# Performance work log

Measured on AMD Instinct MI355X. Metric: run time of the kernel, lower is better.

Reference implementation:

```python
import jax, jax.numpy as jnp
import numpy as np

B, N, DIM = 1, 65536, 256
H, D, G = 8, 64, 64  # heads, dim_head, slice_num


def setup_inputs() -> dict:
    key = jax.random.key(0)
    ks = jax.random.split(key, 16)
    s = 0.02
    return {
        "x": jax.random.normal(ks[0], (B, N, DIM), jnp.float32),
        "Wx": jax.random.normal(ks[1], (H * D, DIM), jnp.float32) * s,
        "bx": jnp.zeros((H * D,), jnp.float32),
        "Wt1": jax.random.normal(ks[2], (G, D), jnp.float32) * s,
        "bt1": jnp.zeros((G,), jnp.float32),
        "Wt2": jax.random.normal(ks[3], (1, G), jnp.float32) * s,
        "bt2": jnp.zeros((1,), jnp.float32),
        "bias": jnp.ones((1, H, 1, 1), jnp.float32) * 0.5,
        "Ws": jax.random.normal(ks[4], (G, D), jnp.float32) * s,
        "bs": jnp.zeros((G,), jnp.float32),
        "Wq": jax.random.normal(ks[5], (D, D), jnp.float32) * s,
        "Wk": jax.random.normal(ks[6], (D, D), jnp.float32) * s,
        "Wv": jax.random.normal(ks[7], (D, D), jnp.float32) * s,
        "Wout": jax.random.normal(ks[8], (DIM, H * D), jnp.float32) * s,
        "bout": jnp.zeros((DIM,), jnp.float32),
        "u": jax.random.uniform(ks[9], (B, H, N, G), jnp.float32),
    }


def _gelu(t):
    return jax.nn.gelu(t, approximate=False)  # torch default exact GELU


def reference(x, Wx, bx, Wt1, bt1, Wt2, bt2, bias, Ws, bs, Wq, Wk, Wv, Wout, bout, u):
    b, n, _ = x.shape
    h, d, g = Wt1.shape[1] and bias.shape[1], Wq.shape[0], Ws.shape[0]
    # project and split heads: b n (h d) -> b h n d
    x_mid = (x @ Wx.T + bx).reshape(b, n, h, d).transpose(0, 2, 1, 3)
    # per-point temperature MLP + learned bias, clamped
    temp = _gelu(_gelu(x_mid @ Wt1.T + bt1) @ Wt2.T + bt2) + bias  # (b,h,n,1)
    temp = jnp.maximum(temp, 0.01)
    # gumbel-softmax slice routing (soft, hard=False)
    logits = x_mid @ Ws.T + bs  # (b,h,n,g)
    gnoise = -jnp.log(-jnp.log(u + 1e-8) + 1e-8)
    slice_weights = jax.nn.softmax((logits + gnoise) / temp, axis=-1)
    norm = slice_weights.sum(axis=2)  # (b,h,g)
    # gather-aggregate points into g slice tokens
    slice_tokens = jnp.einsum('bhnc,bhng->bhgc', x_mid, slice_weights)
    slice_tokens = slice_tokens / (norm[..., None] + 1e-5)
    # tiny g x g attention among slice tokens
    q = slice_tokens @ Wq.T
    k = slice_tokens @ Wk.T
    v = slice_tokens @ Wv.T
    attn = jax.nn.softmax((q @ k.transpose(0, 1, 3, 2)) * (d ** -0.5), axis=-1)
    out_slice = attn @ v  # (b,h,g,d)
    # scatter-combine back to points
    out = jnp.einsum('bhgd,bhng->bhnd', out_slice, slice_weights)
    out = out.transpose(0, 2, 1, 3).reshape(b, n, h * d)
    return out @ Wout.T + bout
```

## Files before the change

### kernel.cpp

```cpp
#include <hip/hip_runtime.h>
#include <math.h>

#define NPTS  65536
#define DIMX  256
#define NH    8
#define HDIM  512

typedef __attribute__((ext_vector_type(4))) float f32x4;
typedef __attribute__((ext_vector_type(8))) short short8;
typedef __attribute__((ext_vector_type(8))) unsigned short ushort8;
typedef __attribute__((ext_vector_type(4))) unsigned short us4;

__device__ __forceinline__ ushort f2bf(float f) {
    unsigned x = __float_as_uint(f);
    return (ushort)((x + 0x7fffu + ((x >> 16) & 1u)) >> 16);
}
__device__ __forceinline__ float bf2f(ushort u) {
    return __uint_as_float((unsigned)u << 16);
}
__device__ __forceinline__ float erf_fast(float x) {
    float ax = fabsf(x);
    float t  = __builtin_amdgcn_rcpf(1.0f + 0.3275911f * ax);
    float p  = fmaf(fmaf(fmaf(fmaf(1.061405429f, t, -1.453152027f), t,
                   1.421413741f), t, -0.284496736f), t, 0.254829592f) * t;
    float y  = 1.0f - p * __expf(-ax * ax);
    return copysignf(y, x);
}
__device__ __forceinline__ float gelu_fast(float x) {
    return 0.5f * x * (1.0f + erf_fast(x * 0.7071067811865476f));
}

__global__ __launch_bounds__(256)
void prep_kernel(const float* __restrict__ Wx, const float* __restrict__ Ws,
                 const float* __restrict__ Wt1,
                 ushort* __restrict__ Wxb, ushort* __restrict__ wb) {
    const int t = threadIdx.x;
    if (blockIdx.x < 64) {
        int idx = blockIdx.x * 2048 + t * 8;
        float4 a0 = *(const float4*)&Wx[idx];
        float4 a1 = *(const float4*)&Wx[idx + 4];
        ushort8 v = { f2bf(a0.x), f2bf(a0.y), f2bf(a0.z), f2bf(a0.w),
                      f2bf(a1.x), f2bf(a1.y), f2bf(a1.z), f2bf(a1.w) };
        *(ushort8*)&Wxb[idx] = v;
    } else {
        int idx = (blockIdx.x - 64) * 2048 + t * 8;
        int row = idx >> 6, col = idx & 63;
        const float* src = (row < 64) ? &Ws[row * 64 + col]
                                      : &Wt1[(row - 64) * 64 + col];
        float4 a0 = *(const float4*)src;
        float4 a1 = *(const float4*)(src + 4);
        ushort8 v = { f2bf(a0.x), f2bf(a0.y), f2bf(a0.z), f2bf(a0.w),
                      f2bf(a1.x), f2bf(a1.y), f2bf(a1.z), f2bf(a1.w) };
        *(ushort8*)&wb[idx] = v;
    }
}

__global__ __launch_bounds__(256)
void gemm_xmid_kernel(const float* __restrict__ A, const ushort* __restrict__ B,
                      const float* __restrict__ bias, ushort* __restrict__ C) {
    __shared__ __align__(16) ushort Al[128][64];
    __shared__ __align__(16) ushort Bl[128][64];
    const int m0 = blockIdx.x * 128, n0 = blockIdx.y * 128;
    const int t = threadIdx.x, l = t & 63, w = t >> 6;
    const int wr = w >> 1, wc = w & 1;
    const int lr = l & 15, lq = l >> 4;

    f32x4 acc[4][4];
    #pragma unroll
    for (int mi = 0; mi < 4; ++mi)
        #pragma unroll
        for (int ni = 0; ni < 4; ++ni) acc[mi][ni] = (f32x4){0.f, 0.f, 0.f, 0.f};

    for (int ks = 0; ks < 4; ++ks) {
        __syncthreads();
        #pragma unroll
        for (int i = 0; i < 4; ++i) {
            int idx = i * 256 + t;
            int row = idx >> 3, g = idx & 7;
            const float* ap = &A[(size_t)(m0 + row) * 256 + ks * 64 + g * 8];
            float4 a0 = *(const float4*)ap;
            float4 a1 = *(const float4*)(ap + 4);
            ushort8 av = { f2bf(a0.x), f2bf(a0.y), f2bf(a0.z), f2bf(a0.w),
                           f2bf(a1.x), f2bf(a1.y), f2bf(a1.z), f2bf(a1.w) };
            *(ushort8*)&Al[row][(g ^ (row & 7)) * 8] = av;
            ushort8 bv = *(const ushort8*)&B[(size_t)(n0 + row) * 256 + ks * 64 + g * 8];
            *(ushort8*)&Bl[row][(g ^ (row & 7)) * 8] = bv;
        }
        __syncthreads();
        #pragma unroll
        for (int kf = 0; kf < 2; ++kf) {
            short8 af[4], bfr[4];
            #pragma unroll
            for (int mi = 0; mi < 4; ++mi) {
                int row = wr * 64 + mi * 16 + lr, g = kf * 4 + lq;
                af[mi] = *(const short8*)&Al[row][(g ^ (row & 7)) * 8];
            }
            #pragma unroll
            for (int ni = 0; ni < 4; ++ni) {
                int row = wc * 64 + ni * 16 + lr, g = kf * 4 + lq;
                bfr[ni] = *(const short8*)&Bl[row][(g ^ (row & 7)) * 8];
            }
            #pragma unroll
            for (int mi = 0; mi < 4; ++mi)
                #pragma unroll
                for (int ni = 0; ni < 4; ++ni)
                    acc[mi][ni] = __builtin_amdgcn_mfma_f32_16x16x32_bf16(
                        af[mi], bfr[ni], acc[mi][ni], 0, 0, 0);
        }
    }
    #pragma unroll
    for (int ni = 0; ni < 4; ++ni) {
        int col = n0 + wc * 64 + ni * 16 + lr;
        float bb = bias[col];
        #pragma unroll
        for (int mi = 0; mi < 4; ++mi)
            #pragma unroll
            for (int j = 0; j < 4; ++j) {
                int row = m0 + wr * 64 + mi * 16 + lq * 4 + j;
                C[(size_t)row * 512 + col] = f2bf(acc[mi][ni][j] + bb);
            }
    }
}

__global__ __launch_bounds__(256)
void lgt1_mfma_kernel(const ushort* __restrict__ xmb,
                      const ushort* __restrict__ wb,
                      const float* __restrict__ bs,  const float* __restrict__ bt1,
                      const float* __restrict__ Wt2, const float* __restrict__ bt2,
                      const float* __restrict__ biasp,
                      const float* __restrict__ u,
                      ushort* __restrict__ swb) {
    __shared__ __align__(16) ushort Al[128][64];
    const int h = blockIdx.y, m0 = blockIdx.x * 128;
    const int t = threadIdx.x, l = t & 63, w = t >> 6;
    const int lr = l & 15, lq = l >> 4;
    const float LOG2E = 1.4426950408889634f;
    const float LN2   = 0.6931471805599453f;
    const float SH2   = 36.0673760222f;

    #pragma unroll
    for (int i = 0; i < 4; ++i) {
        int idx = i * 256 + t;
        int row = idx >> 3, g = idx & 7;
        ushort8 av = *(const ushort8*)&xmb[(size_t)(m0 + row) * 512 + h * 64 + g * 8];
        *(ushort8*)&Al[row][(g ^ (row & 7)) * 8] = av;
    }

    float uu0[4][4];
    #pragma unroll
    for (int jj = 0; jj < 4; ++jj) {
        const int n = m0 + w * 32 + lq * 4 + jj;
        const float* up = &u[((size_t)h * NPTS + n) * 64 + lr];
        #pragma unroll
        for (int ni = 0; ni < 4; ++ni) uu0[jj][ni] = up[ni * 16];
    }
    __syncthreads();

    f32x4 acc[2][8];
    #pragma unroll
    for (int mi = 0; mi < 2; ++mi)
        #pragma unroll
        for (int ni = 0; ni < 8; ++ni) acc[mi][ni] = (f32x4){0.f, 0.f, 0.f, 0.f};

    #pragma unroll
    for (int kf = 0; kf < 2; ++kf) {
        const int g = kf * 4 + lq;
        short8 af[2], bfr[8];
        #pragma unroll
        for (int mi = 0; mi < 2; ++mi) {
            int row = w * 32 + mi * 16 + lr;
            af[mi] = *(const short8*)&Al[row][(g ^ (row & 7)) * 8];
        }
        #pragma unroll
        for (int ni = 0; ni < 8; ++ni)
            bfr[ni] = *(const short8*)&wb[(size_t)(ni * 16 + lr) * 64 + g * 8];
        #pragma unroll
        for (int mi = 0; mi < 2; ++mi)
            #pragma unroll
            for (int ni = 0; ni < 8; ++ni)
                acc[mi][ni] = __builtin_amdgcn_mfma_f32_16x16x32_bf16(
                    af[mi], bfr[ni], acc[mi][ni], 0, 0, 0);
    }

    float uu1[4][4];
    #pragma unroll
    for (int jj = 0; jj < 4; ++jj) {
        const int n = m0 + w * 32 + 16 + lq * 4 + jj;
        const float* up = &u[((size_t)h * NPTS + n) * 64 + lr];
        #pragma unroll
        for (int ni = 0; ni < 4; ++ni) uu1[jj][ni] = up[ni * 16];
    }

    const float bt2v = bt2[0], biasph = biasp[h];
    float bsr[4], bt1r[4], wt2r[4];
    #pragma unroll
    for (int ni = 0; ni < 4; ++ni) {
        bsr[ni]  = bs [ni * 16 + lr];
        bt1r[ni] = bt1[ni * 16 + lr];
        wt2r[ni] = Wt2[ni * 16 + lr];
    }

    #pragma unroll
    for (int mi = 0; mi < 2; ++mi) {
        float ts[4];
        #pragma unroll
        for (int jj = 0; jj < 4; ++jj) {
            float s = 0.f;
            #pragma unroll
            for (int ni = 0; ni < 4; ++ni)
                s += gelu_fast(acc[mi][ni + 4][jj] + bt1r[ni]) * wt2r[ni];
            ts[jj] = s;
        }
        #pragma unroll
        for (int off = 1; off <= 8; off <<= 1) {
            #pragma unroll
            for (int jj = 0; jj < 4; ++jj) ts[jj] += __shfl_xor(ts[jj], off);
        }
        float invt[4], invt2[4];
        #pragma unroll
        for (int jj = 0; jj < 4; ++jj) {
            float tmp = gelu_fast(ts[jj] + bt2v) + biasph;
            tmp = fmaxf(tmp, 0.01f);
            invt[jj]  = __builtin_amdgcn_rcpf(tmp);
            invt2[jj] = invt[jj] * LOG2E;
        }
        float sv[4][4], ps[4] = {0.f, 0.f, 0.f, 0.f};
        #pragma unroll
        for (int jj = 0; jj < 4; ++jj) {
            #pragma unroll
            for (int ni = 0; ni < 4; ++ni) {
                float uuv = (mi == 0 ? uu0[jj][ni] : uu1[jj][ni]);
                float L1 = __log2f(uuv + 1e-8f);
                float inner = fmaf(-LN2, L1, 1e-8f);
                float L2v = __log2f(inner);
                float base = fmaf(acc[mi][ni][jj] + bsr[ni], invt2[jj], -SH2);
                sv[jj][ni] = __builtin_amdgcn_exp2f(fmaf(-invt[jj], L2v, base));
                ps[jj] += sv[jj][ni];
            }
        }
        #pragma unroll
        for (int off = 1; off <= 8; off <<= 1) {
            #pragma unroll
            for (int jj = 0; jj < 4; ++jj) ps[jj] += __shfl_xor(ps[jj], off);
        }
        #pragma unroll
        for (int jj = 0; jj < 4; ++jj) {
            const int n = m0 + w * 32 + mi * 16 + lq * 4 + jj;
            const float inv = __builtin_amdgcn_rcpf(ps[jj]);
            ushort* sp = &swb[(size_t)n * 512 + h * 64 + lr];
            #pragma unroll
            for (int ni = 0; ni < 4; ++ni)
                sp[ni * 16] = f2bf(sv[jj][ni] * inv);
        }
    }
}

__global__ __launch_bounds__(256)
void gather_mfma_kernel(const ushort* __restrict__ xmb, const ushort* __restrict__ swb,
                        float* __restrict__ stp, float* __restrict__ normp) {
    __shared__ __align__(16) ushort tile[2][64][128];
    ushort (* __restrict__ swT)[128] = tile[0];
    ushort (* __restrict__ xT )[128] = tile[1];
    const int h  = blockIdx.y;
    const int n0 = blockIdx.x * 1024;
    const int t  = threadIdx.x, l = t & 63, w = t >> 6;
    const int lr = l & 15, lq = l >> 4;
    const int gb = t & 7;
    const int ng = t >> 3;

    f32x4 acc[4][4];
    #pragma unroll
    for (int gi = 0; gi < 4; ++gi)
        #pragma unroll
        for (int ci = 0; ci < 4; ++ci) acc[gi][ci] = (f32x4){0.f, 0.f, 0.f, 0.f};
    float nrm8[8];
    #pragma unroll
    for (int j = 0; j < 8; ++j) nrm8[j] = 0.f;

    for (int r = 0; r < 8; ++r) {
        const int nt = n0 + r * 128;
        ushort8 sv[4], xv[4];
        #pragma unroll
        for (int i = 0; i < 4; ++i) {
            int n = nt + ng * 4 + i;
            sv[i] = *(const ushort8*)&swb[(size_t)n * 512 + h * 64 + gb * 8];
            xv[i] = *(const ushort8*)&xmb[(size_t)n * 512 + h * 64 + gb * 8];
        }
        __syncthreads();
        #pragma unroll
        for (int j = 0; j < 8; ++j) {
            int g   = gb * 8 + j;
            int swz = (ng >> 1) ^ (g & 7) ^ ((g >> 3) & 7);
            int off = swz * 8 + (ng & 1) * 4;
            us4 s4 = { sv[0][j], sv[1][j], sv[2][j], sv[3][j] };
            us4 x4 = { xv[0][j], xv[1][j], xv[2][j], xv[3][j] };
            *(us4*)&swT[g][off] = s4;
            *(us4*)&xT [g][off] = x4;
            nrm8[j] += (bf2f(sv[0][j]) + bf2f(sv[1][j]))
                     + (bf2f(sv[2][j]) + bf2f(sv[3][j]));
        }
        __syncthreads();
        short8 af[4], bfr[4];
        #pragma unroll
        for (int gi = 0; gi < 4; ++gi) {
            int g   = gi * 16 + lr;
            int swz = (w * 4 + lq) ^ (g & 7) ^ ((g >> 3) & 7);
            af[gi]  = *(const short8*)&swT[g][swz * 8];
            bfr[gi] = *(const short8*)&xT [g][swz * 8];
        }
        #pragma unroll
        for (int gi = 0; gi < 4; ++gi)
            #pragma unroll
            for (int ci = 0; ci < 4; ++ci)
                acc[gi][ci] = __builtin_amdgcn_mfma_f32_16x16x32_bf16(
                    af[gi], bfr[ci], acc[gi][ci], 0, 0, 0);
    }

    float* sred = (float*)tile;
    const size_t stbase = ((size_t)h * 64 + blockIdx.x) * 4096;
    #pragma unroll
    for (int half = 0; half < 2; ++half) {
        __syncthreads();
        #pragma unroll
        for (int gg = 0; gg < 2; ++gg) {
            int gi = half * 2 + gg;
            #pragma unroll
            for (int ci = 0; ci < 4; ++ci)
                #pragma unroll
                for (int j = 0; j < 4; ++j)
                    sred[(w * 32 + gg * 16 + lq * 4 + j) * 64 + ci * 16 + lr]
                        = acc[gi][ci][j];
        }
        __syncthreads();
        #pragma unroll
        for (int i = 0; i < 8; ++i) {
            int e = i * 256 + t;
            float s = (sred[e] + sred[2048 + e]) + (sred[4096 + e] + sred[6144 + e]);
            stp[stbase + half * 2048 + e] = s;
        }
    }

    __syncthreads();
    float* narr = (float*)tile;
    #pragma unroll
    for (int j = 0; j < 8; ++j) narr[ng * 64 + gb * 8 + j] = nrm8[j];
    __syncthreads();
    if (t < 64) {
        float s = 0.f;
        #pragma unroll 8
        for (int k = 0; k < 32; ++k) s += narr[k * 64 + t];
        normp[((size_t)h * 64 + blockIdx.x) * 64 + t] = s;
    }
}

__global__ __launch_bounds__(256)
void reduce_st_kernel(const float* __restrict__ stp, const float* __restrict__ normp,
                      float* __restrict__ st_red, float* __restrict__ nrm) {
    const int h = blockIdx.x;
    const int e = blockIdx.y * 256 + threadIdx.x;
    float s = 0.f;
    #pragma unroll 8
    for (int ch = 0; ch < 64; ++ch)
        s += stp[((size_t)h * 64 + ch) * 4096 + e];
    st_red[(size_t)h * 4096 + e] = s;
    if (blockIdx.y == 0 && threadIdx.x < 64) {
        float ns = 0.f;
        #pragma unroll 8
        for (int ch = 0; ch < 64; ++ch)
            ns += normp[((size_t)h * 64 + ch) * 64 + threadIdx.x];
        nrm[h * 64 + threadIdx.x] = ns + 1e-5f;
    }
}

__global__ __launch_bounds__(256)
void attn_small_kernel(const float* __restrict__ st_red, const float* __restrict__ nrm,
                       const float* __restrict__ Wq, const float* __restrict__ Wk,
                       const float* __restrict__ Wv, float* __restrict__ osl) {
    __shared__ float st[64][68];
    __shared__ float ql[64][68];
    __shared__ float kl[64][68];
    __shared__ float vl[64][68];
    __shared__ float sc[64][68];
    __shared__ float nl[64];
    const int h = blockIdx.x;
    const int t = threadIdx.x;

    if (t < 64) nl[t] = nrm[h * 64 + t];
    __syncthreads();
    for (int e = t; e < 4096; e += 256)
        st[e>>6][e&63] = st_red[(size_t)h * 4096 + e] / nl[e>>6];
    __syncthreads();
    for (int e = t; e < 4096; e += 256) {
        int g = e >> 6, dd = e & 63;
        float aq = 0.f, ak = 0.f, av = 0.f;
        for (int cc = 0; cc < 64; ++cc) {
            float sv = st[g][cc];
            aq = fmaf(sv, Wq[dd*64 + cc], aq);
            ak = fmaf(sv, Wk[dd*64 + cc], ak);
            av = fmaf(sv, Wv[dd*64 + cc], av);
        }
        ql[g][dd] = aq; kl[g][dd] = ak; vl[g][dd] = av;
    }
    __syncthreads();
    for (int e = t; e < 4096; e += 256) {
        int g = e >> 6, gp = e & 63;
        float s = 0.f;
        for (int dd = 0; dd < 64; ++dd) s = fmaf(ql[g][dd], kl[gp][dd], s);
        sc[g][gp] = s * 0.125f;
    }
    __syncthreads();
    if (t < 64) {
        float m = -1e30f;
        for (int j = 0; j < 64; ++j) m = fmaxf(m, sc[t][j]);
        float ssum = 0.f;
        for (int j = 0; j < 64; ++j) { float p = expf(sc[t][j] - m); sc[t][j] = p; ssum += p; }
        float inv = 1.f / ssum;
        for (int j = 0; j < 64; ++j) sc[t][j] *= inv;
    }
    __syncthreads();
    for (int e = t; e < 4096; e += 256) {
        int g = e >> 6, dd = e & 63;
        float s = 0.f;
        for (int gp = 0; gp < 64; ++gp) s = fmaf(sc[g][gp], vl[gp][dd], s);
        osl[(size_t)h * 4096 + e] = s;
    }
}

__global__ __launch_bounds__(256)
void fold_kernel(const float* __restrict__ osl, const float* __restrict__ Wout,
                 ushort* __restrict__ Mtb) {
    __shared__ float os[64][65];
    __shared__ float wl[128][65];
    const int h  = blockIdx.x;
    const int i0 = blockIdx.y * 128;
    const int t  = threadIdx.x;
    for (int e = t; e < 4096; e += 256) os[e>>6][e&63] = osl[(size_t)h * 4096 + e];
    for (int e = t; e < 8192; e += 256) {
        int i = e >> 6, d = e & 63;
        wl[i][d] = Wout[(size_t)(i0 + i) * HDIM + h * 64 + d];
    }
    __syncthreads();
    const int g = t & 63, iq = t >> 6;
    #pragma unroll 4
    for (int k = 0; k < 32; ++k) {
        int i = iq * 32 + k;
        float s = 0.f;
        #pragma unroll
        for (int d = 0; d < 64; ++d) s = fmaf(os[g][d], wl[i][d], s);
        Mtb[(size_t)(i0 + i) * HDIM + h * 64 + g] = f2bf(s);
    }
}

__global__ __launch_bounds__(256)
void gemm_out_kernel(const ushort* __restrict__ A, const ushort* __restrict__ B,
                     const float* __restrict__ bias, float* __restrict__ C) {
    __shared__ __align__(16) ushort Al[128][64];
    __shared__ __align__(16) ushort Bl[128][64];
    const int m0 = blockIdx.x * 128, n0 = blockIdx.y * 128;
    const int t = threadIdx.x, l = t & 63, w = t >> 6;
    const int wr = w >> 1, wc = w & 1;
    const int lr = l & 15, lq = l >> 4;

    f32x4 acc[4][4];
    #pragma unroll
    for (int mi = 0; mi < 4; ++mi)
        #pragma unroll
        for (int ni = 0; ni < 4; ++ni) acc[mi][ni] = (f32x4){0.f, 0.f, 0.f, 0.f};

    for (int ks = 0; ks < 8; ++ks) {
        __syncthreads();
        #pragma unroll
        for (int i = 0; i < 4; ++i) {
            int idx = i * 256 + t;
            int row = idx >> 3, g = idx & 7;
            ushort8 av = *(const ushort8*)&A[(size_t)(m0 + row) * 512 + ks * 64 + g * 8];
            *(ushort8*)&Al[row][(g ^ (row & 7)) * 8] = av;
            ushort8 bv = *(const ushort8*)&B[(size_t)(n0 + row) * 512 + ks * 64 + g * 8];
            *(ushort8*)&Bl[row][(g ^ (row & 7)) * 8] = bv;
        }
        __syncthreads();
        #pragma unroll
        for (int kf = 0; kf < 2; ++kf) {
            short8 af[4], bfr[4];
            #pragma unroll
            for (int mi = 0; mi < 4; ++mi) {
                int row = wr * 64 + mi * 16 + lr, g = kf * 4 + lq;
                af[mi] = *(const short8*)&Al[row][(g ^ (row & 7)) * 8];
            }
            #pragma unroll
            for (int ni = 0; ni < 4; ++ni) {
                int row = wc * 64 + ni * 16 + lr, g = kf * 4 + lq;
                bfr[ni] = *(const short8*)&Bl[row][(g ^ (row & 7)) * 8];
            }
            #pragma unroll
            for (int mi = 0; mi < 4; ++mi)
                #pragma unroll
                for (int ni = 0; ni < 4; ++ni)
                    acc[mi][ni] = __builtin_amdgcn_mfma_f32_16x16x32_bf16(
                        af[mi], bfr[ni], acc[mi][ni], 0, 0, 0);
        }
    }
    #pragma unroll
    for (int ni = 0; ni < 4; ++ni) {
        int col = n0 + wc * 64 + ni * 16 + lr;
        float bb = bias[col];
        #pragma unroll
        for (int mi = 0; mi < 4; ++mi)
            #pragma unroll
            for (int j = 0; j < 4; ++j) {
                int row = m0 + wr * 64 + mi * 16 + lq * 4 + j;
                C[(size_t)row * 256 + col] = acc[mi][ni][j] + bb;
            }
    }
}

extern "C" void kernel_launch(void* const* d_in, const int* in_sizes, int n_in,
                              void* d_out, int out_size, void* d_ws, size_t ws_size,
                              hipStream_t stream) {
    const float* x    = (const float*)d_in[0];
    const float* Wx   = (const float*)d_in[1];
    const float* bx   = (const float*)d_in[2];
    const float* Wt1  = (const float*)d_in[3];
    const float* bt1  = (const float*)d_in[4];
    const float* Wt2  = (const float*)d_in[5];
    const float* bt2  = (const float*)d_in[6];
    const float* biasp= (const float*)d_in[7];
    const float* Ws   = (const float*)d_in[8];
    const float* bs   = (const float*)d_in[9];
    const float* Wq   = (const float*)d_in[10];
    const float* Wk   = (const float*)d_in[11];
    const float* Wv   = (const float*)d_in[12];
    const float* Wout = (const float*)d_in[13];
    const float* bout = (const float*)d_in[14];
    const float* u    = (const float*)d_in[15];
    float* out = (float*)d_out;

    float*  stp    = (float*)d_ws;
    float*  normp  = stp    + (size_t)NH * 64 * 4096;
    float*  st_red = normp  + (size_t)NH * 64 * 64;
    float*  nrm    = st_red + (size_t)NH * 4096;
    float*  osl    = nrm    + (size_t)NH * 64;
    ushort* wb     = (ushort*)(osl + (size_t)NH * 4096);
    ushort* Wxb    = wb  + (size_t)128 * 64;
    ushort* Mtb    = Wxb + (size_t)HDIM * DIMX;
    ushort* xmb    = Mtb + (size_t)DIMX * HDIM;
    ushort* swb    = xmb + (size_t)NPTS * HDIM;

    prep_kernel<<<68, 256, 0, stream>>>(Wx, Ws, Wt1, Wxb, wb);
    gemm_xmid_kernel<<<dim3(512, 4), 256, 0, stream>>>(x, Wxb, bx, xmb);
    lgt1_mfma_kernel<<<dim3(512, 8), 256, 0, stream>>>(xmb, wb, bs, bt1,
                                                       Wt2, bt2, biasp, u, swb);
    gather_mfma_kernel<<<dim3(64, 8), 256, 0, stream>>>(xmb, swb, stp, normp);
    reduce_st_kernel<<<dim3(8, 16), 256, 0, stream>>>(stp, normp, st_red, nrm);
    attn_small_kernel<<<8, 256, 0, stream>>>(st_red, nrm, Wq, Wk, Wv, osl);
    fold_kernel<<<dim3(8, 2), 256, 0, stream>>>(osl, Wout, Mtb);
    gemm_out_kernel<<<dim3(512, 2), 256, 0, stream>>>(swb, Mtb, bout, out);
}
```

Before: 266.0 us.

## Fuse x_mid projection GEMM with slice-logit/temperature kernel via LDS handoff

Merges the x_mid GEMM and the per-head logits/temperature/softmax kernel into one launch. Each block computes a 128x128 x_mid tile (two heads), stages it in LDS, writes it coalesced to global memory, and then runs the second MFMA stage for both heads directly from LDS. This removes the re-read of x_mid from global memory and one kernel launch. The x_mid store also becomes row-coalesced 16-byte writes instead of scattered 2-byte ones. The cost is higher register pressure and fewer blocks in flight for the softmax stage.

```diff
diff --git a/kernel.cpp b/kernel.cpp
--- a/kernel.cpp
+++ b/kernel.cpp
@@ -56,14 +56,23 @@
 }
 
 __global__ __launch_bounds__(256)
-void gemm_xmid_kernel(const float* __restrict__ A, const ushort* __restrict__ B,
-                      const float* __restrict__ bias, ushort* __restrict__ C) {
-    __shared__ __align__(16) ushort Al[128][64];
-    __shared__ __align__(16) ushort Bl[128][64];
-    const int m0 = blockIdx.x * 128, n0 = blockIdx.y * 128;
+void xmid_lgt1_kernel(const float* __restrict__ A, const ushort* __restrict__ B,
+                      const float* __restrict__ bias,
+                      const ushort* __restrict__ wb,
+                      const float* __restrict__ bs,  const float* __restrict__ bt1,
+                      const float* __restrict__ Wt2, const float* __restrict__ bt2,
+                      const float* __restrict__ biasp,
+                      const float* __restrict__ u,
+                      ushort* __restrict__ xmb, ushort* __restrict__ swb) {
+    __shared__ __align__(16) ushort pool[2][128][64];
+    const int hp = blockIdx.y;
+    const int m0 = blockIdx.x * 128, n0 = hp * 128;
     const int t = threadIdx.x, l = t & 63, w = t >> 6;
     const int wr = w >> 1, wc = w & 1;
     const int lr = l & 15, lq = l >> 4;
+    const float LOG2E = 1.4426950408889634f;
+    const float LN2   = 0.6931471805599453f;
+    const float SH2   = 36.0673760222f;
 
     f32x4 acc[4][4];
     #pragma unroll
@@ -82,9 +91,9 @@
             float4 a1 = *(const float4*)(ap + 4);
             ushort8 av = { f2bf(a0.x), f2bf(a0.y), f2bf(a0.z), f2bf(a0.w),
                            f2bf(a1.x), f2bf(a1.y), f2bf(a1.z), f2bf(a1.w) };
-            *(ushort8*)&Al[row][(g ^ (row & 7)) * 8] = av;
+            *(ushort8*)&pool[0][row][(g ^ (row & 7)) * 8] = av;
             ushort8 bv = *(const ushort8*)&B[(size_t)(n0 + row) * 256 + ks * 64 + g * 8];
-            *(ushort8*)&Bl[row][(g ^ (row & 7)) * 8] = bv;
+            *(ushort8*)&pool[1][row][(g ^ (row & 7)) * 8] = bv;
         }
         __syncthreads();
         #pragma unroll
@@ -93,12 +102,12 @@
             #pragma unroll
             for (int mi = 0; mi < 4; ++mi) {
                 int row = wr * 64 + mi * 16 + lr, g = kf * 4 + lq;
-                af[mi] = *(const short8*)&Al[row][(g ^ (row & 7)) * 8];
+                af[mi] = *(const short8*)&pool[0][row][(g ^ (row & 7)) * 8];
             }
             #pragma unroll
             for (int ni = 0; ni < 4; ++ni) {
                 int row = wc * 64 + ni * 16 + lr, g = kf * 4 + lq;
-                bfr[ni] = *(const short8*)&Bl[row][(g ^ (row & 7)) * 8];
+                bfr[ni] = *(const short8*)&pool[1][row][(g ^ (row & 7)) * 8];
             }
             #pragma unroll
             for (int mi = 0; mi < 4; ++mi)
@@ -108,90 +117,32 @@
                         af[mi], bfr[ni], acc[mi][ni], 0, 0, 0);
         }
     }
+
+    __syncthreads();
+    ushort (* __restrict__ Xl)[128] = (ushort (*)[128])(&pool[0][0][0]);
     #pragma unroll
     for (int ni = 0; ni < 4; ++ni) {
-        int col = n0 + wc * 64 + ni * 16 + lr;
-        float bb = bias[col];
+        int colL = wc * 64 + ni * 16 + lr;
+        float bb = bias[n0 + colL];
+        int gg = colL >> 3, c7 = colL & 7;
         #pragma unroll
         for (int mi = 0; mi < 4; ++mi)
             #pragma unroll
             for (int j = 0; j < 4; ++j) {
-                int row = m0 + wr * 64 + mi * 16 + lq * 4 + j;
-                C[(size_t)row * 512 + col] = f2bf(acc[mi][ni][j] + bb);
-            }
-    }
-}
-
-__global__ __launch_bounds__(256)
-void lgt1_mfma_kernel(const ushort* __restrict__ xmb,
-                      const ushort* __restrict__ wb,
-                      const float* __restrict__ bs,  const float* __restrict__ bt1,
-                      const float* __restrict__ Wt2, const float* __restrict__ bt2,
-                      const float* __restrict__ biasp,
-                      const float* __restrict__ u,
-                      ushort* __restrict__ swb) {
-    __shared__ __align__(16) ushort Al[128][64];
-    const int h = blockIdx.y, m0 = blockIdx.x * 128;
-    const int t = threadIdx.x, l = t & 63, w = t >> 6;
-    const int lr = l & 15, lq = l >> 4;
-    const float LOG2E = 1.4426950408889634f;
-    const float LN2   = 0.6931471805599453f;
-    const float SH2   = 36.0673760222f;
-
-    #pragma unroll
-    for (int i = 0; i < 4; ++i) {
-        int idx = i * 256 + t;
-        int row = idx >> 3, g = idx & 7;
-        ushort8 av = *(const ushort8*)&xmb[(size_t)(m0 + row) * 512 + h * 64 + g * 8];
-        *(ushort8*)&Al[row][(g ^ (row & 7)) * 8] = av;
-    }
-
-    float uu0[4][4];
-    #pragma unroll
-    for (int jj = 0; jj < 4; ++jj) {
-        const int n = m0 + w * 32 + lq * 4 + jj;
-        const float* up = &u[((size_t)h * NPTS + n) * 64 + lr];
-        #pragma unroll
-        for (int ni = 0; ni < 4; ++ni) uu0[jj][ni] = up[ni * 16];
-    }
-    __syncthreads();
-
-    f32x4 acc[2][8];
-    #pragma unroll
-    for (int mi = 0; mi < 2; ++mi)
-        #pragma unroll
-        for (int ni = 0; ni < 8; ++ni) acc[mi][ni] = (f32x4){0.f, 0.f, 0.f, 0.f};
-
-    #pragma unroll
-    for (int kf = 0; kf < 2; ++kf) {
-        const int g = kf * 4 + lq;
-        short8 af[2], bfr[8];
-        #pragma unroll
-        for (int mi = 0; mi < 2; ++mi) {
-            int row = w * 32 + mi * 16 + lr;
-            af[mi] = *(const short8*)&Al[row][(g ^ (row & 7)) * 8];
-        }
-        #pragma unroll
-        for (int ni = 0; ni < 8; ++ni)
-            bfr[ni] = *(const short8*)&wb[(size_t)(ni * 16 + lr) * 64 + g * 8];
-        #pragma unroll
-        for (int mi = 0; mi < 2; ++mi)
-            #pragma unroll
-            for (int ni = 0; ni < 8; ++ni)
-                acc[mi][ni] = __builtin_amdgcn_mfma_f32_16x16x32_bf16(
-                    af[mi], bfr[ni], acc[mi][ni], 0, 0, 0);
-    }
-
-    float uu1[4][4];
-    #pragma unroll
-    for (int jj = 0; jj < 4; ++jj) {
-        const int n = m0 + w * 32 + 16 + lq * 4 + jj;
-        const float* up = &u[((size_t)h * NPTS + n) * 64 + lr];
-        #pragma unroll
-        for (int ni = 0; ni < 4; ++ni) uu1[jj][ni] = up[ni * 16];
-    }
-
-    const float bt2v = bt2[0], biasph = biasp[h];
+                int row = wr * 64 + mi * 16 + lq * 4 + j;
+                Xl[row][(gg ^ (row & 7)) * 8 + c7] = f2bf(acc[mi][ni][j] + bb);
+            }
+    }
+    __syncthreads();
+    #pragma unroll
+    for (int i = 0; i < 8; ++i) {
+        int e = i * 256 + t;
+        int row = e >> 4, gg = e & 15;
+        ushort8 v = *(const ushort8*)&Xl[row][(gg ^ (row & 7)) * 8];
+        *(ushort8*)&xmb[(size_t)(m0 + row) * 512 + n0 + gg * 8] = v;
+    }
+
+    const float bt2v = bt2[0];
     float bsr[4], bt1r[4], wt2r[4];
     #pragma unroll
     for (int ni = 0; ni < 4; ++ni) {
@@ -201,56 +152,96 @@
     }
 
     #pragma unroll
-    for (int mi = 0; mi < 2; ++mi) {
-        float ts[4];
-        #pragma unroll
-        for (int jj = 0; jj < 4; ++jj) {
-            float s = 0.f;
-            #pragma unroll
-            for (int ni = 0; ni < 4; ++ni)
-                s += gelu_fast(acc[mi][ni + 4][jj] + bt1r[ni]) * wt2r[ni];
-            ts[jj] = s;
-        }
-        #pragma unroll
-        for (int off = 1; off <= 8; off <<= 1) {
-            #pragma unroll
-            for (int jj = 0; jj < 4; ++jj) ts[jj] += __shfl_xor(ts[jj], off);
-        }
-        float invt[4], invt2[4];
-        #pragma unroll
-        for (int jj = 0; jj < 4; ++jj) {
-            float tmp = gelu_fast(ts[jj] + bt2v) + biasph;
-            tmp = fmaxf(tmp, 0.01f);
-            invt[jj]  = __builtin_amdgcn_rcpf(tmp);
-            invt2[jj] = invt[jj] * LOG2E;
-        }
-        float sv[4][4], ps[4] = {0.f, 0.f, 0.f, 0.f};
-        #pragma unroll
-        for (int jj = 0; jj < 4; ++jj) {
-            #pragma unroll
-            for (int ni = 0; ni < 4; ++ni) {
-                float uuv = (mi == 0 ? uu0[jj][ni] : uu1[jj][ni]);
-                float L1 = __log2f(uuv + 1e-8f);
-                float inner = fmaf(-LN2, L1, 1e-8f);
-                float L2v = __log2f(inner);
-                float base = fmaf(acc[mi][ni][jj] + bsr[ni], invt2[jj], -SH2);
-                sv[jj][ni] = __builtin_amdgcn_exp2f(fmaf(-invt[jj], L2v, base));
-                ps[jj] += sv[jj][ni];
-            }
-        }
-        #pragma unroll
-        for (int off = 1; off <= 8; off <<= 1) {
-            #pragma unroll
-            for (int jj = 0; jj < 4; ++jj) ps[jj] += __shfl_xor(ps[jj], off);
-        }
-        #pragma unroll
-        for (int jj = 0; jj < 4; ++jj) {
-            const int n = m0 + w * 32 + mi * 16 + lq * 4 + jj;
-            const float inv = __builtin_amdgcn_rcpf(ps[jj]);
-            ushort* sp = &swb[(size_t)n * 512 + h * 64 + lr];
-            #pragma unroll
-            for (int ni = 0; ni < 4; ++ni)
-                sp[ni * 16] = f2bf(sv[jj][ni] * inv);
+    for (int hh = 0; hh < 2; ++hh) {
+        const int h = hp * 2 + hh;
+        const float biasph = biasp[h];
+
+        f32x4 acc2[2][8];
+        #pragma unroll
+        for (int mi = 0; mi < 2; ++mi)
+            #pragma unroll
+            for (int ni = 0; ni < 8; ++ni) acc2[mi][ni] = (f32x4){0.f, 0.f, 0.f, 0.f};
+
+        #pragma unroll
+        for (int kf = 0; kf < 2; ++kf) {
+            const int g = kf * 4 + lq;
+            short8 af[2], bfr[8];
+            #pragma unroll
+            for (int mi = 0; mi < 2; ++mi) {
+                int row = w * 32 + mi * 16 + lr;
+                int gg = hh * 8 + g;
+                af[mi] = *(const short8*)&Xl[row][(gg ^ (row & 7)) * 8];
+            }
+            #pragma unroll
+            for (int ni = 0; ni < 8; ++ni)
+                bfr[ni] = *(const short8*)&wb[(size_t)(ni * 16 + lr) * 64 + g * 8];
+            #pragma unroll
+            for (int mi = 0; mi < 2; ++mi)
+                #pragma unroll
+                for (int ni = 0; ni < 8; ++ni)
+                    acc2[mi][ni] = __builtin_amdgcn_mfma_f32_16x16x32_bf16(
+                        af[mi], bfr[ni], acc2[mi][ni], 0, 0, 0);
+        }
+
+        #pragma unroll
+        for (int mi = 0; mi < 2; ++mi) {
+            float uu[4][4];
+            #pragma unroll
+            for (int jj = 0; jj < 4; ++jj) {
+                const int n = m0 + w * 32 + mi * 16 + lq * 4 + jj;
+                const float* up = &u[((size_t)h * NPTS + n) * 64 + lr];
+                #pragma unroll
+                for (int ni = 0; ni < 4; ++ni) uu[jj][ni] = up[ni * 16];
+            }
+            float ts[4];
+            #pragma unroll
+            for (int jj = 0; jj < 4; ++jj) {
+                float s = 0.f;
+                #pragma unroll
+                for (int ni = 0; ni < 4; ++ni)
+                    s += gelu_fast(acc2[mi][ni + 4][jj] + bt1r[ni]) * wt2r[ni];
+                ts[jj] = s;
+            }
+            #pragma unroll
+            for (int off = 1; off <= 8; off <<= 1) {
+                #pragma unroll
+                for (int jj = 0; jj < 4; ++jj) ts[jj] += __shfl_xor(ts[jj], off);
+            }
+            float invt[4], invt2[4];
+            #pragma unroll
+            for (int jj = 0; jj < 4; ++jj) {
+                float tmp = gelu_fast(ts[jj] + bt2v) + biasph;
+                tmp = fmaxf(tmp, 0.01f);
+                invt[jj]  = __builtin_amdgcn_rcpf(tmp);
+                invt2[jj] = invt[jj] * LOG2E;
+            }
+            float sv[4][4], ps[4] = {0.f, 0.f, 0.f, 0.f};
+            #pragma unroll
+            for (int jj = 0; jj < 4; ++jj) {
+                #pragma unroll
+                for (int ni = 0; ni < 4; ++ni) {
+                    float L1 = __log2f(uu[jj][ni] + 1e-8f);
+                    float inner = fmaf(-LN2, L1, 1e-8f);
+                    float L2v = __log2f(inner);
+                    float base = fmaf(acc2[mi][ni][jj] + bsr[ni], invt2[jj], -SH2);
+                    sv[jj][ni] = __builtin_amdgcn_exp2f(fmaf(-invt[jj], L2v, base));
+                    ps[jj] += sv[jj][ni];
+                }
+            }
+            #pragma unroll
+            for (int off = 1; off <= 8; off <<= 1) {
+                #pragma unroll
+                for (int jj = 0; jj < 4; ++jj) ps[jj] += __shfl_xor(ps[jj], off);
+            }
+            #pragma unroll
+            for (int jj = 0; jj < 4; ++jj) {
+                const int n = m0 + w * 32 + mi * 16 + lq * 4 + jj;
+                const float inv = __builtin_amdgcn_rcpf(ps[jj]);
+                ushort* sp = &swb[(size_t)n * 512 + h * 64 + lr];
+                #pragma unroll
+                for (int ni = 0; ni < 4; ++ni)
+                    sp[ni * 16] = f2bf(sv[jj][ni] * inv);
+            }
         }
     }
 }
@@ -547,9 +538,9 @@
     ushort* swb    = xmb + (size_t)NPTS * HDIM;
 
     prep_kernel<<<68, 256, 0, stream>>>(Wx, Ws, Wt1, Wxb, wb);
-    gemm_xmid_kernel<<<dim3(512, 4), 256, 0, stream>>>(x, Wxb, bx, xmb);
-    lgt1_mfma_kernel<<<dim3(512, 8), 256, 0, stream>>>(xmb, wb, bs, bt1,
-                                                       Wt2, bt2, biasp, u, swb);
+    xmid_lgt1_kernel<<<dim3(512, 4), 256, 0, stream>>>(x, Wxb, bx, wb, bs, bt1,
+                                                       Wt2, bt2, biasp, u,
+                                                       xmb, swb);
     gather_mfma_kernel<<<dim3(64, 8), 256, 0, stream>>>(xmb, swb, stp, normp);
     reduce_st_kernel<<<dim3(8, 16), 256, 0, stream>>>(stp, normp, st_red, nrm);
     attn_small_kernel<<<8, 256, 0, stream>>>(st_red, nrm, Wq, Wk, Wv, osl);
```

Result: no change. 263.1 us (-1.1%).
